# Performance work log

Measured on AMD Instinct MI355X. Metric: run time of the kernel, lower is better.

The kernel has to match this reference:

```python
import jax, jax.numpy as jnp
import numpy as np
from jax import lax

B, C, H, W = 8, 256, 64, 64
O, K, E = 256, 3, 3  # out_channels, kernel_size, num_experts

def setup_inputs() -> dict:
    key = jax.random.key(0)
    k1, k2, k3, k4, k5 = jax.random.split(key, 5)
    q = jax.random.normal(k1, (B, C, H, W), dtype=jnp.float32)
    y = jax.random.normal(k2, (B, C, H, W), dtype=jnp.float32)
    experts = jax.random.normal(k3, (E, O, 2 * C, K, K), dtype=jnp.float32)
    # torch nn.Linear(2C, E): store transposed [2C, E] for ctx @ gate_w
    bound = 1.0 / np.sqrt(2 * C)
    gate_w = jax.random.uniform(k4, (2 * C, E), minval=-bound, maxval=bound, dtype=jnp.float32)
    gate_b = jax.random.uniform(k5, (E,), minval=-bound, maxval=bound, dtype=jnp.float32)
    return {"q": q, "y": y, "experts": experts, "gate_w": gate_w, "gate_b": gate_b}

def reference(q, y, experts, gate_w, gate_b):
    # gate: softmax over experts from global-avg-pooled context of y (duplicated)
    y_ctx = jnp.mean(y, axis=(2, 3))                       # [B, C]
    context = jnp.concatenate([y_ctx, y_ctx], axis=1)       # [B, 2C]
    gates = jax.nn.softmax(context @ gate_w + gate_b, axis=1)  # [B, E]
    # per-sample fused kernel: sum_e gates[b,e] * experts[e]  -> [B, O, 2C, K, K]
    w = jnp.einsum('be,eoikl->boikl', gates, experts)
    xy = jnp.concatenate([q, q], axis=1)                     # [B, 2C, H, W]
    # batched dynamic conv via grouped conv: batch -> groups (no Python loop)
    b, c2, h, wd = xy.shape
    x1 = xy.reshape(1, b * c2, h, wd)
    w1 = w.reshape(b * O, c2, K, K)
    out = lax.conv_general_dilated(
        x1, w1, window_strides=(1, 1), padding='SAME',
        dimension_numbers=('NCHW', 'OIHW', 'NCHW'),
        feature_group_count=b)
    return out.reshape(b, O, h, wd)
```

## Files before the change

kernel.cpp:

```cpp
#include <hip/hip_runtime.h>
#include <hip/hip_bf16.h>
#include <math.h>


typedef __bf16 bf16x8 __attribute__((ext_vector_type(8)));
typedef float f32x4 __attribute__((ext_vector_type(4)));

#define AS1 __attribute__((address_space(1)))
#define AS3 __attribute__((address_space(3)))

__global__ __launch_bounds__(64) void yctx_kernel(const float* __restrict__ y,
                                                  float* __restrict__ yctx) {
  int bc = blockIdx.x;
  const float4* p = (const float4*)(y + (size_t)bc * 4096);
  int lane = threadIdx.x;
  float s = 0.f;
  for (int i = lane; i < 1024; i += 64) {
    float4 v = p[i];
    s += v.x + v.y + v.z + v.w;
  }
#pragma unroll
  for (int off = 32; off > 0; off >>= 1) s += __shfl_down(s, off, 64);
  if (lane == 0) yctx[bc] = s * (1.f / 4096.f);
}

__global__ __launch_bounds__(64) void logits_kernel(const float* __restrict__ yctx,
                                                    const float* __restrict__ gw,
                                                    const float* __restrict__ gb,
                                                    float* __restrict__ logits) {
  int be = blockIdx.x;
  int b = be / 3, e = be - b * 3;
  int lane = threadIdx.x;
  float s = 0.f;
  for (int c = lane; c < 256; c += 64)
    s += yctx[b * 256 + c] * (gw[c * 3 + e] + gw[(c + 256) * 3 + e]);
#pragma unroll
  for (int off = 32; off > 0; off >>= 1) s += __shfl_down(s, off, 64);
  if (lane == 0) logits[be] = s + gb[e];
}

__global__ __launch_bounds__(64) void wbuild_kernel(const float* __restrict__ experts,
                                                    const float* __restrict__ logits,
                                                    __bf16* __restrict__ wf) {
  int bid = blockIdx.x;
  int o = bid >> 3, ch = bid & 7;
  int t = threadIdx.x;
  int cl = t & 31, half = t >> 5;
  float g[8][3];
#pragma unroll
  for (int b = 0; b < 8; b++) {
    float l0 = logits[b * 3 + 0], l1 = logits[b * 3 + 1], l2 = logits[b * 3 + 2];
    float m = fmaxf(l0, fmaxf(l1, l2));
    float e0 = __expf(l0 - m), e1 = __expf(l1 - m), e2 = __expf(l2 - m);
    float inv = 1.f / (e0 + e1 + e2);
    g[b][0] = e0 * inv; g[b][1] = e1 * inv; g[b][2] = e2 * inv;
  }
  int c = ch * 32 + cl + half * 256;
  int clp = (((cl >> 3) ^ ((o >> 1) & 3)) << 3) | (cl & 7);
#pragma unroll 1
  for (int tap = 0; tap < 9; tap++) {
    float v[3];
#pragma unroll
    for (int e = 0; e < 3; e++)
      v[e] = experts[(((size_t)e * 256 + o) * 512 + c) * 9 + tap];
    float s[3];
#pragma unroll
    for (int e = 0; e < 3; e++)
      s[e] = v[e] + __shfl_xor(v[e], 32, 64);
    if (half == 0) {
#pragma unroll
      for (int b = 0; b < 8; b++) {
        float val = g[b][0] * s[0] + g[b][1] * s[1] + g[b][2] * s[2];
        wf[((((size_t)b * 9 + tap) * 8 + ch) * 256 + o) * 32 + clp] = (__bf16)val;
      }
    }
  }
}

__global__ __launch_bounds__(256) void qt_kernel(const float* __restrict__ q,
                                                 __bf16* __restrict__ qT) {
  int bid = blockIdx.x;
  int hp = bid % 66;
  int t2 = bid / 66;
  int ch = t2 & 7;
  int b = t2 >> 3;
  __bf16* dst = qT + (((size_t)(b * 8 + ch) * 66 + hp) * 66) * 32;
  int tid = threadIdx.x;
  if (hp == 0 || hp == 65) {
    for (int i = tid; i < 66 * 32; i += 256) dst[i] = (__bf16)0.f;
    return;
  }
  __shared__ float tile[32][65];
  int h = hp - 1;
  {
    int w = tid & 63, ci = tid >> 6;
#pragma unroll
    for (int j = 0; j < 8; j++) {
      int c = ci * 8 + j;
      tile[c][w] = q[(((size_t)b * 256 + ch * 32 + c) * 64 + h) * 64 + w];
    }
  }
  __syncthreads();
  int cl = tid & 31, wsl = tid >> 5;
  if (tid < 32) dst[tid] = (__bf16)0.f;
  else if (tid < 64) dst[65 * 32 + (tid - 32)] = (__bf16)0.f;
#pragma unroll
  for (int k = 0; k < 8; k++) {
    int w = wsl * 8 + k;
    int wp = w + 1;
    int clp = (((cl >> 3) ^ ((wp >> 1) & 3)) << 3) | (cl & 7);
    dst[wp * 32 + clp] = (__bf16)tile[cl][w];
  }
}

__global__ __launch_bounds__(256) void conv_kernel(const __bf16* __restrict__ qT,
                                                   const __bf16* __restrict__ wf,
                                                   float* __restrict__ out) {
  __shared__ __align__(16) __bf16 Alds[128 * 32];
  __shared__ __align__(16) __bf16 Qlds[4 * 66 * 32];
  const int tid = threadIdx.x;
  const int lane = tid & 63;
  const int wv = tid >> 6;
  const int wm = wv >> 1, wn = wv & 1;
  const int l15 = lane & 15, qd = lane >> 4;

  const int bid = blockIdx.x;
  const int b = bid >> 6;
  const int rem = bid & 63;
  const int o0 = (rem >> 5) * 128;
  const int h0 = (rem & 31) * 2;

  f32x4 acc[4][4];
  {
    f32x4 z = {0.f, 0.f, 0.f, 0.f};
#pragma unroll
    for (int i = 0; i < 4; i++)
#pragma unroll
      for (int j = 0; j < 4; j++) acc[i][j] = z;
  }

  int aoff[4];
#pragma unroll
  for (int mi = 0; mi < 4; mi++) {
    int orow = wm * 64 + mi * 16 + l15;
    int g = (qd ^ ((l15 >> 1) & 3)) << 3;
    aoff[mi] = (orow * 32 + g) * 2;
  }

  const char* qT_b = (const char*)qT + (size_t)b * 8 * 66 * 66 * 32 * 2;

#pragma unroll 1
  for (int ch = 0; ch < 8; ch++) {
    __syncthreads();
    const char* qsrc = qT_b + ((size_t)ch * 66 + h0) * 66 * 32 * 2;
    for (int i = tid; i < 1056; i += 256) {
      int ub = i - lane;
      __builtin_amdgcn_global_load_lds(
          (const AS1 void*)(qsrc + ((size_t)i << 4)),
          (AS3 void*)((char*)Qlds + ((size_t)ub << 4)), 16, 0, 0);
    }
#pragma unroll 1
    for (int tap = 0; tap < 9; tap++) {
      if (tap) __syncthreads();
      const char* asrc = (const char*)wf +
          (((((size_t)b * 9 + tap) * 8 + ch) * 256 + o0) * 32) * 2;
      for (int i = tid; i < 512; i += 256) {
        int ub = i - lane;
        __builtin_amdgcn_global_load_lds(
            (const AS1 void*)(asrc + ((size_t)i << 4)),
            (AS3 void*)((char*)Alds + ((size_t)ub << 4)), 16, 0, 0);
      }
      __syncthreads();

      const int dh = tap / 3, dw = tap - dh * 3;
      const int r = wn + dh;
      bf16x8 af[4];
#pragma unroll
      for (int mi = 0; mi < 4; mi++)
        af[mi] = *(const bf16x8*)((const char*)Alds + aoff[mi]);
#pragma unroll
      for (int ni = 0; ni < 4; ni++) {
        int wp = ni * 16 + l15 + dw;
        int g = (qd ^ ((wp >> 1) & 3)) << 3;
        bf16x8 bfv = *(const bf16x8*)((const char*)Qlds +
                                      ((r * 66 + wp) * 32 + g) * 2);
#pragma unroll
        for (int mi = 0; mi < 4; mi++)
          acc[mi][ni] = __builtin_amdgcn_mfma_f32_16x16x32_bf16(
              af[mi], bfv, acc[mi][ni], 0, 0, 0);
      }
    }
  }

  const int hh = h0 + wn;
#pragma unroll
  for (int mi = 0; mi < 4; mi++) {
    int o = o0 + wm * 64 + mi * 16 + qd * 4;
#pragma unroll
    for (int ni = 0; ni < 4; ni++) {
      int w = ni * 16 + l15;
#pragma unroll
      for (int rr = 0; rr < 4; rr++)
        out[(((size_t)b * 256 + (o + rr)) * 64 + hh) * 64 + w] = acc[mi][ni][rr];
    }
  }
}

extern "C" void kernel_launch(void* const* d_in, const int* in_sizes, int n_in,
                              void* d_out, int out_size, void* d_ws, size_t ws_size,
                              hipStream_t stream) {
  (void)in_sizes; (void)n_in; (void)out_size; (void)ws_size;
  const float* q = (const float*)d_in[0];
  const float* y = (const float*)d_in[1];
  const float* experts = (const float*)d_in[2];
  const float* gate_w = (const float*)d_in[3];
  const float* gate_b = (const float*)d_in[4];
  float* out = (float*)d_out;

  char* ws = (char*)d_ws;
  float* yctx = (float*)ws;
  float* logits = (float*)(ws + 8192);
  __bf16* wf = (__bf16*)(ws + 16384);
  __bf16* qT = (__bf16*)(ws + 16384 + 9437184);

  yctx_kernel<<<2048, 64, 0, stream>>>(y, yctx);
  logits_kernel<<<24, 64, 0, stream>>>(yctx, gate_w, gate_b, logits);
  qt_kernel<<<8 * 8 * 66, 256, 0, stream>>>(q, qT);
  wbuild_kernel<<<2048, 64, 0, stream>>>(experts, logits, wf);
  conv_kernel<<<512, 256, 0, stream>>>(qT, wf, out);
}
```

Baseline: 187.5 us.

## Double-buffer conv LDS loads and restructure weight build and q transpose

The conv kernel now double-buffers both the weight tile and the q tile in LDS. The next tap's weights and the next channel chunk's input rows are prefetched with global_load_lds while MFMAs run on the current buffers, which leaves one barrier per tap. The weight build kernel stages each output channel's expert slices in shared memory with coalesced float4 loads, so it no longer does strided per-tap global reads. The q transpose writes vectorized bf16x4 stores. The cost is twice the LDS per conv block, which may lower occupancy, and correctness now depends on barrier placement across the prefetches.

Result: no change. 186.3 us (-0.6%).

```diff
diff --git a/kernel.cpp b/kernel.cpp
--- a/kernel.cpp
+++ b/kernel.cpp
@@ -4,6 +4,7 @@
 
 
 typedef __bf16 bf16x8 __attribute__((ext_vector_type(8)));
+typedef __bf16 bf16x4 __attribute__((ext_vector_type(4)));
 typedef float f32x4 __attribute__((ext_vector_type(4)));
 
 #define AS1 __attribute__((address_space(1)))
@@ -39,40 +40,44 @@
   if (lane == 0) logits[be] = s + gb[e];
 }
 
-__global__ __launch_bounds__(64) void wbuild_kernel(const float* __restrict__ experts,
-                                                    const float* __restrict__ logits,
-                                                    __bf16* __restrict__ wf) {
-  int bid = blockIdx.x;
-  int o = bid >> 3, ch = bid & 7;
-  int t = threadIdx.x;
-  int cl = t & 31, half = t >> 5;
-  float g[8][3];
-#pragma unroll
-  for (int b = 0; b < 8; b++) {
-    float l0 = logits[b * 3 + 0], l1 = logits[b * 3 + 1], l2 = logits[b * 3 + 2];
+__global__ __launch_bounds__(256) void wbuild_kernel(const float* __restrict__ experts,
+                                                     const float* __restrict__ logits,
+                                                     __bf16* __restrict__ wf) {
+  int o = blockIdx.x;
+  int tid = threadIdx.x;
+  __shared__ float sf[3][2304];
+  __shared__ float g[8][3];
+
+#pragma unroll
+  for (int e = 0; e < 3; e++) {
+    const float4* src = (const float4*)(experts + ((size_t)e * 256 + o) * 4608);
+    float4* dstp = (float4*)sf[e];
+    for (int i = tid; i < 576; i += 256) {
+      float4 a = src[i], bq = src[i + 576];
+      float4 r;
+      r.x = a.x + bq.x; r.y = a.y + bq.y; r.z = a.z + bq.z; r.w = a.w + bq.w;
+      dstp[i] = r;
+    }
+  }
+  if (tid < 8) {
+    float l0 = logits[tid * 3 + 0], l1 = logits[tid * 3 + 1], l2 = logits[tid * 3 + 2];
     float m = fmaxf(l0, fmaxf(l1, l2));
     float e0 = __expf(l0 - m), e1 = __expf(l1 - m), e2 = __expf(l2 - m);
     float inv = 1.f / (e0 + e1 + e2);
-    g[b][0] = e0 * inv; g[b][1] = e1 * inv; g[b][2] = e2 * inv;
-  }
-  int c = ch * 32 + cl + half * 256;
+    g[tid][0] = e0 * inv; g[tid][1] = e1 * inv; g[tid][2] = e2 * inv;
+  }
+  __syncthreads();
+
+  int cl = tid & 31, ch = tid >> 5;
   int clp = (((cl >> 3) ^ ((o >> 1) & 3)) << 3) | (cl & 7);
 #pragma unroll 1
-  for (int tap = 0; tap < 9; tap++) {
-    float v[3];
-#pragma unroll
-    for (int e = 0; e < 3; e++)
-      v[e] = experts[(((size_t)e * 256 + o) * 512 + c) * 9 + tap];
-    float s[3];
-#pragma unroll
-    for (int e = 0; e < 3; e++)
-      s[e] = v[e] + __shfl_xor(v[e], 32, 64);
-    if (half == 0) {
-#pragma unroll
-      for (int b = 0; b < 8; b++) {
-        float val = g[b][0] * s[0] + g[b][1] * s[1] + g[b][2] * s[2];
-        wf[((((size_t)b * 9 + tap) * 8 + ch) * 256 + o) * 32 + clp] = (__bf16)val;
-      }
+  for (int b = 0; b < 8; b++) {
+    float g0 = g[b][0], g1 = g[b][1], g2 = g[b][2];
+#pragma unroll
+    for (int tap = 0; tap < 9; tap++) {
+      float v = g0 * sf[0][tid * 9 + tap] + g1 * sf[1][tid * 9 + tap] +
+                g2 * sf[2][tid * 9 + tap];
+      wf[((((size_t)b * 9 + tap) * 8 + ch) * 256 + o) * 32 + clp] = (__bf16)v;
     }
   }
 }
@@ -86,38 +91,44 @@
   int b = t2 >> 3;
   __bf16* dst = qT + (((size_t)(b * 8 + ch) * 66 + hp) * 66) * 32;
   int tid = threadIdx.x;
+  float4 z4 = {0.f, 0.f, 0.f, 0.f};
   if (hp == 0 || hp == 65) {
-    for (int i = tid; i < 66 * 32; i += 256) dst[i] = (__bf16)0.f;
+    float4* d4 = (float4*)dst;
+    for (int i = tid; i < 264; i += 256) d4[i] = z4;
     return;
   }
-  __shared__ float tile[32][65];
+  __shared__ float tile2[64][33];
   int h = hp - 1;
   {
     int w = tid & 63, ci = tid >> 6;
 #pragma unroll
     for (int j = 0; j < 8; j++) {
       int c = ci * 8 + j;
-      tile[c][w] = q[(((size_t)b * 256 + ch * 32 + c) * 64 + h) * 64 + w];
-    }
-  }
+      tile2[w][c] = q[(((size_t)b * 256 + ch * 32 + c) * 64 + h) * 64 + w];
+    }
+  }
+  if (tid < 4) ((float4*)dst)[tid] = z4;
+  else if (tid < 8) ((float4*)(dst + 65 * 32))[tid - 4] = z4;
   __syncthreads();
-  int cl = tid & 31, wsl = tid >> 5;
-  if (tid < 32) dst[tid] = (__bf16)0.f;
-  else if (tid < 64) dst[65 * 32 + (tid - 32)] = (__bf16)0.f;
-#pragma unroll
-  for (int k = 0; k < 8; k++) {
-    int w = wsl * 8 + k;
-    int wp = w + 1;
-    int clp = (((cl >> 3) ^ ((wp >> 1) & 3)) << 3) | (cl & 7);
-    dst[wp * 32 + clp] = (__bf16)tile[cl][w];
+
+  int a = tid & 7, wsl = tid >> 3;
+  int cl4 = a * 4;
+#pragma unroll
+  for (int k = 0; k < 2; k++) {
+    int w = wsl * 2 + k, wp = w + 1;
+    int clp4 = (((cl4 >> 3) ^ ((wp >> 1) & 3)) << 3) | (cl4 & 7);
+    float v0 = tile2[w][cl4 + 0], v1 = tile2[w][cl4 + 1];
+    float v2 = tile2[w][cl4 + 2], v3 = tile2[w][cl4 + 3];
+    bf16x4 r = {(__bf16)v0, (__bf16)v1, (__bf16)v2, (__bf16)v3};
+    *(bf16x4*)(dst + wp * 32 + clp4) = r;
   }
 }
 
 __global__ __launch_bounds__(256) void conv_kernel(const __bf16* __restrict__ qT,
                                                    const __bf16* __restrict__ wf,
                                                    float* __restrict__ out) {
-  __shared__ __align__(16) __bf16 Alds[128 * 32];
-  __shared__ __align__(16) __bf16 Qlds[4 * 66 * 32];
+  __shared__ __align__(16) __bf16 Alds[2][128 * 32];
+  __shared__ __align__(16) __bf16 Qlds[2][4 * 66 * 32];
   const int tid = threadIdx.x;
   const int lane = tid & 63;
   const int wv = tid >> 6;
@@ -148,47 +159,74 @@
   }
 
   const char* qT_b = (const char*)qT + (size_t)b * 8 * 66 * 66 * 32 * 2;
-
+  const char* wf_b = (const char*)wf + (size_t)b * 9 * 8 * 256 * 32 * 2;
+
+  {
+    const char* qsrc = qT_b + ((size_t)h0) * 66 * 32 * 2;
+    for (int i = tid; i < 1056; i += 256) {
+      int ub = i - lane;
+      __builtin_amdgcn_global_load_lds((const AS1 void*)(qsrc + ((size_t)i << 4)),
+                                       (AS3 void*)((char*)Qlds[0] + ((size_t)ub << 4)),
+                                       16, 0, 0);
+    }
+    const char* asrc = wf_b + ((size_t)o0) * 32 * 2;
+    for (int i = tid; i < 512; i += 256) {
+      int ub = i - lane;
+      __builtin_amdgcn_global_load_lds((const AS1 void*)(asrc + ((size_t)i << 4)),
+                                       (AS3 void*)((char*)Alds[0] + ((size_t)ub << 4)),
+                                       16, 0, 0);
+    }
+    __syncthreads();
+  }
+
+  int s = 0;
 #pragma unroll 1
   for (int ch = 0; ch < 8; ch++) {
-    __syncthreads();
-    const char* qsrc = qT_b + ((size_t)ch * 66 + h0) * 66 * 32 * 2;
-    for (int i = tid; i < 1056; i += 256) {
-      int ub = i - lane;
-      __builtin_amdgcn_global_load_lds(
-          (const AS1 void*)(qsrc + ((size_t)i << 4)),
-          (AS3 void*)((char*)Qlds + ((size_t)ub << 4)), 16, 0, 0);
-    }
+    int dh = 0, dw = 0;
 #pragma unroll 1
-    for (int tap = 0; tap < 9; tap++) {
-      if (tap) __syncthreads();
-      const char* asrc = (const char*)wf +
-          (((((size_t)b * 9 + tap) * 8 + ch) * 256 + o0) * 32) * 2;
-      for (int i = tid; i < 512; i += 256) {
-        int ub = i - lane;
-        __builtin_amdgcn_global_load_lds(
-            (const AS1 void*)(asrc + ((size_t)i << 4)),
-            (AS3 void*)((char*)Alds + ((size_t)ub << 4)), 16, 0, 0);
+    for (int tap = 0; tap < 9; tap++, s++) {
+      if (s < 71) {
+        int tapn = (tap == 8) ? 0 : tap + 1;
+        int chn = (tap == 8) ? ch + 1 : ch;
+        const char* asrc = wf_b + (((size_t)(tapn * 8 + chn) * 256 + o0) * 32) * 2;
+        char* adst = (char*)Alds[(s + 1) & 1];
+        for (int i = tid; i < 512; i += 256) {
+          int ub = i - lane;
+          __builtin_amdgcn_global_load_lds((const AS1 void*)(asrc + ((size_t)i << 4)),
+                                           (AS3 void*)(adst + ((size_t)ub << 4)),
+                                           16, 0, 0);
+        }
       }
-      __syncthreads();
-
-      const int dh = tap / 3, dw = tap - dh * 3;
+      if (tap == 4 && ch < 7) {
+        const char* qsrc = qT_b + ((size_t)(ch + 1) * 66 + h0) * 66 * 32 * 2;
+        char* qdst = (char*)Qlds[(ch + 1) & 1];
+        for (int i = tid; i < 1056; i += 256) {
+          int ub = i - lane;
+          __builtin_amdgcn_global_load_lds((const AS1 void*)(qsrc + ((size_t)i << 4)),
+                                           (AS3 void*)(qdst + ((size_t)ub << 4)),
+                                           16, 0, 0);
+        }
+      }
+
+      const char* Ab = (const char*)Alds[s & 1];
+      const char* Qb = (const char*)Qlds[ch & 1];
       const int r = wn + dh;
       bf16x8 af[4];
 #pragma unroll
       for (int mi = 0; mi < 4; mi++)
-        af[mi] = *(const bf16x8*)((const char*)Alds + aoff[mi]);
+        af[mi] = *(const bf16x8*)(Ab + aoff[mi]);
 #pragma unroll
       for (int ni = 0; ni < 4; ni++) {
         int wp = ni * 16 + l15 + dw;
         int g = (qd ^ ((wp >> 1) & 3)) << 3;
-        bf16x8 bfv = *(const bf16x8*)((const char*)Qlds +
-                                      ((r * 66 + wp) * 32 + g) * 2);
+        bf16x8 bfv = *(const bf16x8*)(Qb + ((r * 66 + wp) * 32 + g) * 2);
 #pragma unroll
         for (int mi = 0; mi < 4; mi++)
           acc[mi][ni] = __builtin_amdgcn_mfma_f32_16x16x32_bf16(
               af[mi], bfv, acc[mi][ni], 0, 0, 0);
       }
+      __syncthreads();
+      if (++dw == 3) { dw = 0; ++dh; }
     }
   }
 
@@ -226,6 +264,6 @@
   yctx_kernel<<<2048, 64, 0, stream>>>(y, yctx);
   logits_kernel<<<24, 64, 0, stream>>>(yctx, gate_w, gate_b, logits);
   qt_kernel<<<8 * 8 * 66, 256, 0, stream>>>(q, qT);
-  wbuild_kernel<<<2048, 64, 0, stream>>>(experts, logits, wf);
+  wbuild_kernel<<<256, 256, 0, stream>>>(experts, logits, wf);
   conv_kernel<<<512, 256, 0, stream>>>(qT, wf, out);
 }
```
